# Performance work log

Measured on AMD Instinct MI355X. Metric: run time of the kernel, lower is better.

## Reference

```python
import jax, jax.numpy as jnp
import numpy as np

TIM_SIZE, TIM_EMB = 48, 64
APP_SIZE, APP_EMB = 10000, 256
UID_SIZE, UID_EMB = 10000, 256
INPUT_SIZE = TIM_EMB + APP_EMB  # 320
S = 4096
N = S - 3  # windows of length 4


def setup_inputs() -> dict:
    key = jax.random.key(0)
    ks = jax.random.split(key, 12)
    inp = {
        "tim": jax.random.randint(ks[0], (S, 1), 0, TIM_SIZE),
        "app": jax.random.uniform(ks[1], (S, APP_SIZE), dtype=jnp.float32),
        "loc": jax.random.randint(ks[2], (S, 1), 0, 1),
        "uid": jax.random.randint(ks[3], (1,), 0, UID_SIZE),
        "ptim": jax.random.randint(ks[4], (N, 1), 0, TIM_SIZE),
        # learned parameters
        "emb_tim_w": jax.random.normal(ks[5], (TIM_SIZE, TIM_EMB), dtype=jnp.float32) * 0.02,
        "emb_uid_w": jax.random.normal(ks[6], (UID_SIZE, UID_EMB), dtype=jnp.float32) * 0.02,
        "emb_app_w": jax.random.normal(ks[7], (APP_SIZE, APP_EMB), dtype=jnp.float32) * 0.02,
        "attn_W": jax.random.uniform(ks[8], (INPUT_SIZE, 1), dtype=jnp.float32),
        "attn_b": jax.random.uniform(ks[9], (4, 1), dtype=jnp.float32),
        "attn_fc_w": jax.random.normal(ks[10], (APP_EMB, INPUT_SIZE), dtype=jnp.float32) * 0.02,
        "attn_fc_b": jnp.zeros((APP_EMB,), dtype=jnp.float32),
        "dec_w": jax.random.normal(ks[11], (APP_SIZE, APP_EMB + TIM_EMB), dtype=jnp.float32) * 0.02,
        "dec_b": jnp.zeros((APP_SIZE,), dtype=jnp.float32),
    }
    return inp


def reference(tim, app, loc, uid, ptim, emb_tim_w, emb_uid_w, emb_app_w,
              attn_W, attn_b, attn_fc_w, attn_fc_b, dec_w, dec_b):
    # embeddings (squeeze(1) in torch)
    tim_emb = emb_tim_w[tim[:, 0]]    # [S, TIM_EMB]
    ptim_emb = emb_tim_w[ptim[:, 0]]  # [N, TIM_EMB]
    # 'sum' app embedding mode: multi-hot @ table
    app_emb = app @ emb_app_w         # [S, APP_EMB]
    x = jnp.concatenate([app_emb, tim_emb], axis=1)  # [S, INPUT_SIZE]; dropout is identity at eval
    # sliding windows of length 4 (vectorizes the torch per-i loop)
    n = tim.shape[0] - 3
    idx = jnp.arange(n)[:, None] + jnp.arange(4)[None, :]  # [N, 4]
    win = x[idx]                                          # [N, 4, INPUT_SIZE]
    H = jnp.tanh(win @ attn_W + attn_b)                   # [N, 4, 1]
    Xn = H / jnp.sum(jnp.abs(H), axis=(1, 2), keepdims=True)  # L1 normalize over the window
    pooled = jnp.einsum('nf,nfd->nd', Xn[:, :, 0], win)   # [N, INPUT_SIZE]
    out = pooled @ attn_fc_w.T + attn_fc_b                # [N, APP_EMB]
    uid_emb = emb_uid_w[uid[0]]                           # [APP_EMB], broadcast = repeat
    out = out * uid_emb
    out = jnp.concatenate([out, ptim_emb], axis=1)        # [N, APP_EMB+TIM_EMB]
    score = jax.nn.sigmoid(out @ dec_w.T + dec_b)         # [N, APP_SIZE]
    return score
```

## Files before the change

kernel.cpp:

```cpp
#include <hip/hip_runtime.h>

typedef __attribute__((ext_vector_type(8))) short  bf16x8;
typedef __attribute__((ext_vector_type(8))) unsigned short u16x8;
typedef __attribute__((ext_vector_type(4))) float  f32x4;

constexpr int S    = 4096;
constexpr int NR   = 4093;
constexpr int KAPP = 10000;
constexpr int EAPP = 256;
constexpr int ETIM = 64;
constexpr int DIN  = 320;
constexpr int NDEC = 10000;
constexpr int NSK  = 10;
constexpr int KCH  = 1024;
constexpr int KPAD = NSK * KCH;
constexpr int NS   = KCH / 32;
constexpr int LDP  = 40;
constexpr int LDA2 = 328;

__device__ inline unsigned short f2bf(float f) {
    unsigned u = __float_as_uint(f);
    u += 0x7fffu + ((u >> 16) & 1u);
    return (unsigned short)(u >> 16);
}
__device__ inline float bf2f(unsigned short h) {
    return __uint_as_float(((unsigned)h) << 16);
}
__device__ inline u16x8 pack8(f32x4 a, f32x4 b) {
    u16x8 v;
    v[0]=f2bf(a.x); v[1]=f2bf(a.y); v[2]=f2bf(a.z); v[3]=f2bf(a.w);
    v[4]=f2bf(b.x); v[5]=f2bf(b.y); v[6]=f2bf(b.z); v[7]=f2bf(b.w);
    return v;
}
__device__ inline bf16x8 as_bf(u16x8 v) {
    union { u16x8 u; bf16x8 b; } c; c.u = v; return c.b;
}

__global__ __launch_bounds__(256) void k_cvt_bf16(
    const float* __restrict__ in, unsigned short* __restrict__ out, int n8)
{
    int id = blockIdx.x * 256 + threadIdx.x;
    if (id >= n8) return;
    const float* p = in + (size_t)id * 8;
    f32x4 a = *reinterpret_cast<const f32x4*>(p);
    f32x4 b = *reinterpret_cast<const f32x4*>(p + 4);
    *reinterpret_cast<u16x8*>(out + (size_t)id * 8) = pack8(a, b);
}

__global__ __launch_bounds__(256) void k_transpose_appw(
    const float* __restrict__ B, unsigned short* __restrict__ Bp)
{
    __shared__ float T[64][68];
    const int kt = blockIdx.x * 64, nt = blockIdx.y * 64;
    const int tid = threadIdx.x;
    #pragma unroll
    for (int i = 0; i < 4; ++i) {
        int c = tid + (i << 8);
        int k = c >> 4, n4 = (c & 15) << 2;
        f32x4 v = {0.f, 0.f, 0.f, 0.f};
        if (kt + k < KAPP)
            v = *reinterpret_cast<const f32x4*>(&B[(size_t)(kt + k) * EAPP + nt + n4]);
        *reinterpret_cast<f32x4*>(&T[k][n4]) = v;
    }
    __syncthreads();
    #pragma unroll
    for (int i = 0; i < 2; ++i) {
        int c = tid + (i << 8);
        int n = c >> 3, ko = (c & 7) << 3;
        u16x8 v;
        #pragma unroll
        for (int j = 0; j < 8; ++j) v[j] = f2bf(T[ko + j][n]);
        *reinterpret_cast<u16x8*>(&Bp[(size_t)(nt + n) * KPAD + kt + ko]) = v;
    }
}

__global__ __launch_bounds__(256) void k_embed_tim(
    const int* __restrict__ tim, const float* __restrict__ emb_tim,
    unsigned short* __restrict__ xb)
{
    int r = blockIdx.x * 4 + (threadIdx.x >> 6);
    int e = threadIdx.x & 63;
    xb[(size_t)r * DIN + EAPP + e] = f2bf(emb_tim[tim[r] * ETIM + e]);
}
__global__ __launch_bounds__(256) void k_embed_ptim(
    const int* __restrict__ ptim, const float* __restrict__ emb_tim,
    unsigned short* __restrict__ yb)
{
    int r = blockIdx.x * 4 + (threadIdx.x >> 6);
    int e = threadIdx.x & 63;
    if (r < NR) yb[(size_t)r * DIN + EAPP + e] = f2bf(emb_tim[ptim[r] * ETIM + e]);
}

__global__ __launch_bounds__(256, 3) void k_app(
    const float* __restrict__ A, const unsigned short* __restrict__ Bp,
    float* __restrict__ part)
{
    __shared__ unsigned short As[2][64 * LDP];
    __shared__ unsigned short Bs[2][256 * LDP];
    const int tid = threadIdx.x, lane = tid & 63, w = tid >> 6;
    const int ks = blockIdx.x, bm = blockIdx.y << 6;
    const int wc = w << 6, rl = lane & 15, kh8 = (lane >> 4) << 3;
    const int k0 = ks * KCH;
    const int arow = tid >> 2, ak0 = (tid & 3) << 3;

    u16x8 ra, rb[4];
    auto gload = [&](int step) {
        const int kt = k0 + (step << 5);
        {
            const int k = kt + ak0;
            u16x8 v = {0,0,0,0,0,0,0,0};
            if (k < KAPP) {
                const float* p = &A[(size_t)(bm + arow) * KAPP + k];
                v = pack8(*reinterpret_cast<const f32x4*>(p),
                          *reinterpret_cast<const f32x4*>(p + 4));
            }
            ra = v;
        }
        #pragma unroll
        for (int i = 0; i < 4; ++i) {
            int c = tid + (i << 8);
            int row = c >> 2, ko = (c & 3) << 3;
            rb[i] = *reinterpret_cast<const u16x8*>(&Bp[(size_t)row * KPAD + kt + ko]);
        }
    };
    auto swrite = [&](int b) {
        *reinterpret_cast<u16x8*>(&As[b][arow * LDP + ak0]) = ra;
        #pragma unroll
        for (int i = 0; i < 4; ++i) {
            int c = tid + (i << 8);
            int row = c >> 2, ko = (c & 3) << 3;
            *reinterpret_cast<u16x8*>(&Bs[b][row * LDP + ko]) = rb[i];
        }
    };

    f32x4 acc[4][4];
    #pragma unroll
    for (int i = 0; i < 4; ++i)
        #pragma unroll
        for (int j = 0; j < 4; ++j) acc[i][j] = (f32x4){0.f, 0.f, 0.f, 0.f};

    gload(0); swrite(0); __syncthreads();
    for (int t = 0; t < NS; ++t) {
        const int cur = t & 1;
        const bool more = (t + 1 < NS);
        if (more) gload(t + 1);
        bf16x8 af[4], bfr[4];
        #pragma unroll
        for (int i = 0; i < 4; ++i)
            af[i] = *reinterpret_cast<const bf16x8*>(
                &As[cur][(i * 16 + rl) * LDP + kh8]);
        #pragma unroll
        for (int j = 0; j < 4; ++j)
            bfr[j] = *reinterpret_cast<const bf16x8*>(
                &Bs[cur][(wc + j * 16 + rl) * LDP + kh8]);
        #pragma unroll
        for (int i = 0; i < 4; ++i)
            #pragma unroll
            for (int j = 0; j < 4; ++j)
                acc[i][j] = __builtin_amdgcn_mfma_f32_16x16x32_bf16(
                    af[i], bfr[j], acc[i][j], 0, 0, 0);
        if (more) swrite(cur ^ 1);
        __syncthreads();
    }

    float* P = part + ((size_t)ks * S + bm) * EAPP;
    const int rq = (lane >> 4) << 2;
    #pragma unroll
    for (int i = 0; i < 4; ++i)
        #pragma unroll
        for (int j = 0; j < 4; ++j) {
            int col = wc + j * 16 + rl;
            #pragma unroll
            for (int q = 0; q < 4; ++q)
                P[(size_t)(i * 16 + rq + q) * EAPP + col] = acc[i][j][q];
        }
}

__global__ __launch_bounds__(256) void k_reduce_app(
    const float* __restrict__ part, unsigned short* __restrict__ xb)
{
    int id = blockIdx.x * 256 + threadIdx.x;
    int row = id >> 6, c4 = (id & 63) << 2;
    f32x4 s = {0.f, 0.f, 0.f, 0.f};
    #pragma unroll
    for (int sl = 0; sl < NSK; ++sl) {
        f32x4 v = *reinterpret_cast<const f32x4*>(
            &part[((size_t)sl * S + row) * EAPP + c4]);
        s.x += v.x; s.y += v.y; s.z += v.z; s.w += v.w;
    }
    unsigned short* o = &xb[(size_t)row * DIN + c4];
    o[0] = f2bf(s.x); o[1] = f2bf(s.y); o[2] = f2bf(s.z); o[3] = f2bf(s.w);
}

__global__ __launch_bounds__(256) void k_score(
    const unsigned short* __restrict__ xb, const float* __restrict__ W,
    float* __restrict__ s)
{
    int wv = threadIdx.x >> 6, lane = threadIdx.x & 63;
    int m = blockIdx.x * 4 + wv;
    float sum = 0.f;
    #pragma unroll
    for (int i = 0; i < 5; ++i) {
        int k = lane + (i << 6);
        sum += bf2f(xb[(size_t)m * DIN + k]) * W[k];
    }
    #pragma unroll
    for (int off = 32; off; off >>= 1) sum += __shfl_down(sum, off);
    if (lane == 0) s[m] = sum;
}

__global__ void k_pooled(
    const unsigned short* __restrict__ xb, const float* __restrict__ s,
    const float* __restrict__ attn_b, unsigned short* __restrict__ pooledb)
{
    int n = blockIdx.x, d = threadIdx.x;
    float h[4], den = 0.f;
    #pragma unroll
    for (int f = 0; f < 4; ++f) {
        h[f] = tanhf(s[n + f] + attn_b[f]);
        den += fabsf(h[f]);
    }
    float inv = 1.f / den, p = 0.f;
    #pragma unroll
    for (int f = 0; f < 4; ++f)
        p = fmaf(h[f] * inv, bf2f(xb[(size_t)(n + f) * DIN + d]), p);
    pooledb[(size_t)n * DIN + d] = f2bf(p);
}

template<int EPI>
__global__ __launch_bounds__(256, 3) void k_nt320(
    const unsigned short* __restrict__ A, const unsigned short* __restrict__ B,
    int Nb, int Mlim,
    const float* __restrict__ bias,
    const float* __restrict__ emb_uid, const int* __restrict__ uid,
    void* __restrict__ Cout, int ldc)
{
    __shared__ unsigned short As[64 * LDA2];
    const int tid = threadIdx.x, lane = tid & 63, w = tid >> 6;
    const int qx = gridDim.x >> 3;
    const int swz = (blockIdx.x & 7) * qx + (blockIdx.x >> 3);
    const int bm = (swz & 63) << 6, bn = (swz >> 6) << 8;
    const int rl = lane & 15, kh8 = (lane >> 4) << 3;
    const int wc = w << 6;

    {
        const int row = tid >> 2, c0 = tid & 3;
        const unsigned short* src = A + (size_t)(bm + row) * DIN;
        unsigned short* dst = As + row * LDA2;
        #pragma unroll
        for (int t = 0; t < 10; ++t) {
            int ch = (c0 + (t << 2)) << 3;
            *reinterpret_cast<u16x8*>(dst + ch) =
                *reinterpret_cast<const u16x8*>(src + ch);
        }
    }
    __syncthreads();

    f32x4 acc[4][4];
    #pragma unroll
    for (int i = 0; i < 4; ++i)
        #pragma unroll
        for (int j = 0; j < 4; ++j) acc[i][j] = (f32x4){0.f, 0.f, 0.f, 0.f};

    u16x8 b0[4], b1[4];
#define LOADB(DST, KSN) do {                                                    \
    const int kg_ = ((KSN) << 5) + kh8;                                         \
    _Pragma("unroll")                                                           \
    for (int j = 0; j < 4; ++j) {                                               \
        int brow = bn + wc + j * 16 + rl;                                       \
        u16x8 v_ = {0,0,0,0,0,0,0,0};                                           \
        if (brow < Nb)                                                          \
            v_ = *reinterpret_cast<const u16x8*>(&B[(size_t)brow * DIN + kg_]); \
        DST[j] = v_;                                                            \
    }                                                                           \
} while (0)

#define STEPNT(BARR, KSN) do {                                                  \
    const int kg_ = ((KSN) << 5) + kh8;                                         \
    bf16x8 af_[4];                                                              \
    _Pragma("unroll")                                                           \
    for (int i = 0; i < 4; ++i)                                                 \
        af_[i] = *reinterpret_cast<const bf16x8*>(                              \
            &As[(i * 16 + rl) * LDA2 + kg_]);                                   \
    _Pragma("unroll")                                                           \
    for (int i = 0; i < 4; ++i)                                                 \
        _Pragma("unroll")                                                       \
        for (int j = 0; j < 4; ++j)                                             \
            acc[i][j] = __builtin_amdgcn_mfma_f32_16x16x32_bf16(                \
                af_[i], as_bf(BARR[j]), acc[i][j], 0, 0, 0);                     \
} while (0)

    LOADB(b0, 0);
    #pragma unroll
    for (int p = 0; p < 5; ++p) {
        LOADB(b1, 2 * p + 1);
        STEPNT(b0, 2 * p);
        if (2 * p + 2 < 10) LOADB(b0, 2 * p + 2);
        STEPNT(b1, 2 * p + 1);
    }
#undef LOADB
#undef STEPNT

    const int rq = (lane >> 4) << 2;
    if (EPI == 1) {
        unsigned short* C = (unsigned short*)Cout;
        const float* us = emb_uid + (size_t)uid[0] * EAPP;
        #pragma unroll
        for (int j = 0; j < 4; ++j) {
            int col = bn + wc + j * 16 + rl;
            if (col >= Nb) continue;
            float um = us[col], bb = bias[col];
            #pragma unroll
            for (int i = 0; i < 4; ++i)
                #pragma unroll
                for (int q = 0; q < 4; ++q) {
                    int row = bm + i * 16 + rq + q;
                    if (row < Mlim)
                        C[(size_t)row * ldc + col] = f2bf((acc[i][j][q] + bb) * um);
                }
        }
    } else {
        float* C = (float*)Cout;
        #pragma unroll
        for (int j = 0; j < 4; ++j) {
            int col = bn + wc + j * 16 + rl;
            if (col >= Nb) continue;
            float bb = bias[col];
            #pragma unroll
            for (int i = 0; i < 4; ++i)
                #pragma unroll
                for (int q = 0; q < 4; ++q) {
                    int row = bm + i * 16 + rq + q;
                    if (row < Mlim) {
                        float v = acc[i][j][q] + bb;
                        C[(size_t)row * ldc + col] = 1.f / (1.f + __expf(-v));
                    }
                }
        }
    }
}

extern "C" void kernel_launch(void* const* d_in, const int* in_sizes, int n_in,
                              void* d_out, int out_size, void* d_ws, size_t ws_size,
                              hipStream_t stream)
{
    const int*   tim       = (const int*)  d_in[0];
    const float* app       = (const float*)d_in[1];
    const int*   uid       = (const int*)  d_in[3];
    const int*   ptim      = (const int*)  d_in[4];
    const float* emb_tim_w = (const float*)d_in[5];
    const float* emb_uid_w = (const float*)d_in[6];
    const float* emb_app_w = (const float*)d_in[7];
    const float* attn_W    = (const float*)d_in[8];
    const float* attn_b    = (const float*)d_in[9];
    const float* attn_fc_w = (const float*)d_in[10];
    const float* attn_fc_b = (const float*)d_in[11];
    const float* dec_w     = (const float*)d_in[12];
    const float* dec_b     = (const float*)d_in[13];
    float* out = (float*)d_out;

    char* w = (char*)d_ws;
    size_t o = 0;
    auto alloc = [&](size_t bytes) { char* p = w + o; o = (o + bytes + 511) & ~(size_t)511; return p; };
    unsigned short* xb      = (unsigned short*)alloc((size_t)S * DIN * 2);
    unsigned short* pooledb = (unsigned short*)alloc((size_t)S * DIN * 2);
    unsigned short* yb      = (unsigned short*)alloc((size_t)S * DIN * 2);
    float*          s       = (float*)        alloc((size_t)S * 4);
    unsigned short* Bp      = (unsigned short*)alloc((size_t)EAPP * KPAD * 2);
    unsigned short* decb    = (unsigned short*)alloc((size_t)NDEC * DIN * 2);
    unsigned short* fcb     = (unsigned short*)alloc((size_t)EAPP * DIN * 2);
    float*          part    = (float*)        alloc((size_t)NSK * S * EAPP * 4);

    k_cvt_bf16<<<(NDEC * DIN / 8 + 255) / 256, 256, 0, stream>>>(dec_w, decb, NDEC * DIN / 8);
    k_cvt_bf16<<<(EAPP * DIN / 8 + 255) / 256, 256, 0, stream>>>(attn_fc_w, fcb, EAPP * DIN / 8);
    dim3 gT(KPAD / 64, EAPP / 64);
    k_transpose_appw<<<gT, 256, 0, stream>>>(emb_app_w, Bp);
    k_embed_tim<<<S / 4, 256, 0, stream>>>(tim, emb_tim_w, xb);

    dim3 gApp(NSK, S / 64);
    k_app<<<gApp, 256, 0, stream>>>(app, Bp, part);
    k_reduce_app<<<S * 64 / 256, 256, 0, stream>>>(part, xb);

    k_score<<<S / 4, 256, 0, stream>>>(xb, attn_W, s);
    k_pooled<<<NR, DIN, 0, stream>>>(xb, s, attn_b, pooledb);
    k_embed_ptim<<<S / 4, 256, 0, stream>>>(ptim, emb_tim_w, yb);

    k_nt320<1><<<64, 256, 0, stream>>>(pooledb, fcb, EAPP, S,
                                       attn_fc_b, emb_uid_w, uid, yb, DIN);
    k_nt320<2><<<40 * 64, 256, 0, stream>>>(yb, decb, NDEC, NR,
                                            dec_b, nullptr, nullptr, out, NDEC);
}
```

Before: 248.8 us.

## Use k-chunk-major LDS layout, rebalance split-K, raise occupancy bounds

Replaces the padded row-major LDS tiles in the app GEMM and the 320-wide NT GEMM with a layout where each 8-element k-chunk is stored contiguously across rows. MFMA fragment reads then become conflict-free sequential 16-byte accesses, and the padding is no longer needed. The app GEMM split-K changes from 10x1024 to 8x1280, which cuts the number of partial sums to reduce. Both kernels raise launch_bounds min-blocks from 3 to 4, and the NT kernel prefetches B two steps ahead. The higher occupancy target may force register spills.

```diff
diff --git a/kernel.cpp b/kernel.cpp
--- a/kernel.cpp
+++ b/kernel.cpp
@@ -11,12 +11,10 @@
 constexpr int ETIM = 64;
 constexpr int DIN  = 320;
 constexpr int NDEC = 10000;
-constexpr int NSK  = 10;
-constexpr int KCH  = 1024;
+constexpr int NSK  = 8;
+constexpr int KCH  = 1280;
 constexpr int KPAD = NSK * KCH;
 constexpr int NS   = KCH / 32;
-constexpr int LDP  = 40;
-constexpr int LDA2 = 328;
 
 __device__ inline unsigned short f2bf(float f) {
     unsigned u = __float_as_uint(f);
@@ -91,23 +89,23 @@
     if (r < NR) yb[(size_t)r * DIN + EAPP + e] = f2bf(emb_tim[ptim[r] * ETIM + e]);
 }
 
-__global__ __launch_bounds__(256, 3) void k_app(
+__global__ __launch_bounds__(256, 4) void k_app(
     const float* __restrict__ A, const unsigned short* __restrict__ Bp,
     float* __restrict__ part)
 {
-    __shared__ unsigned short As[2][64 * LDP];
-    __shared__ unsigned short Bs[2][256 * LDP];
+    __shared__ unsigned short As[2][4 * 64 * 8];
+    __shared__ unsigned short Bs[2][4 * 256 * 8];
     const int tid = threadIdx.x, lane = tid & 63, w = tid >> 6;
     const int ks = blockIdx.x, bm = blockIdx.y << 6;
-    const int wc = w << 6, rl = lane & 15, kh8 = (lane >> 4) << 3;
+    const int wc = w << 6, rl = lane & 15, kq = lane >> 4;
     const int k0 = ks * KCH;
-    const int arow = tid >> 2, ak0 = (tid & 3) << 3;
+    const int arow = tid >> 2, ac = tid & 3;
 
     u16x8 ra, rb[4];
     auto gload = [&](int step) {
         const int kt = k0 + (step << 5);
         {
-            const int k = kt + ak0;
+            const int k = kt + (ac << 3);
             u16x8 v = {0,0,0,0,0,0,0,0};
             if (k < KAPP) {
                 const float* p = &A[(size_t)(bm + arow) * KAPP + k];
@@ -119,17 +117,18 @@
         #pragma unroll
         for (int i = 0; i < 4; ++i) {
             int c = tid + (i << 8);
-            int row = c >> 2, ko = (c & 3) << 3;
-            rb[i] = *reinterpret_cast<const u16x8*>(&Bp[(size_t)row * KPAD + kt + ko]);
+            int row = c >> 2, ck = c & 3;
+            rb[i] = *reinterpret_cast<const u16x8*>(
+                &Bp[(size_t)row * KPAD + kt + (ck << 3)]);
         }
     };
     auto swrite = [&](int b) {
-        *reinterpret_cast<u16x8*>(&As[b][arow * LDP + ak0]) = ra;
+        *reinterpret_cast<u16x8*>(&As[b][((ac << 6) + arow) << 3]) = ra;
         #pragma unroll
         for (int i = 0; i < 4; ++i) {
             int c = tid + (i << 8);
-            int row = c >> 2, ko = (c & 3) << 3;
-            *reinterpret_cast<u16x8*>(&Bs[b][row * LDP + ko]) = rb[i];
+            int row = c >> 2, ck = c & 3;
+            *reinterpret_cast<u16x8*>(&Bs[b][((ck << 8) + row) << 3]) = rb[i];
         }
     };
 
@@ -148,11 +147,11 @@
         #pragma unroll
         for (int i = 0; i < 4; ++i)
             af[i] = *reinterpret_cast<const bf16x8*>(
-                &As[cur][(i * 16 + rl) * LDP + kh8]);
+                &As[cur][((kq << 6) + i * 16 + rl) << 3]);
         #pragma unroll
         for (int j = 0; j < 4; ++j)
             bfr[j] = *reinterpret_cast<const bf16x8*>(
-                &Bs[cur][(wc + j * 16 + rl) * LDP + kh8]);
+                &Bs[cur][((kq << 8) + wc + j * 16 + rl) << 3]);
         #pragma unroll
         for (int i = 0; i < 4; ++i)
             #pragma unroll
@@ -164,7 +163,7 @@
     }
 
     float* P = part + ((size_t)ks * S + bm) * EAPP;
-    const int rq = (lane >> 4) << 2;
+    const int rq = kq << 2;
     #pragma unroll
     for (int i = 0; i < 4; ++i)
         #pragma unroll
@@ -228,30 +227,29 @@
 }
 
 template<int EPI>
-__global__ __launch_bounds__(256, 3) void k_nt320(
+__global__ __launch_bounds__(256, 4) void k_nt320(
     const unsigned short* __restrict__ A, const unsigned short* __restrict__ B,
     int Nb, int Mlim,
     const float* __restrict__ bias,
     const float* __restrict__ emb_uid, const int* __restrict__ uid,
     void* __restrict__ Cout, int ldc)
 {
-    __shared__ unsigned short As[64 * LDA2];
+    __shared__ unsigned short As[40 * 64 * 8];
     const int tid = threadIdx.x, lane = tid & 63, w = tid >> 6;
     const int qx = gridDim.x >> 3;
     const int swz = (blockIdx.x & 7) * qx + (blockIdx.x >> 3);
     const int bm = (swz & 63) << 6, bn = (swz >> 6) << 8;
-    const int rl = lane & 15, kh8 = (lane >> 4) << 3;
+    const int rl = lane & 15, kq = lane >> 4;
     const int wc = w << 6;
 
     {
         const int row = tid >> 2, c0 = tid & 3;
         const unsigned short* src = A + (size_t)(bm + row) * DIN;
-        unsigned short* dst = As + row * LDA2;
         #pragma unroll
         for (int t = 0; t < 10; ++t) {
-            int ch = (c0 + (t << 2)) << 3;
-            *reinterpret_cast<u16x8*>(dst + ch) =
-                *reinterpret_cast<const u16x8*>(src + ch);
+            int ck = c0 + (t << 2);
+            *reinterpret_cast<u16x8*>(&As[((ck << 6) + row) << 3]) =
+                *reinterpret_cast<const u16x8*>(src + (ck << 3));
         }
     }
     __syncthreads();
@@ -264,7 +262,7 @@
 
     u16x8 b0[4], b1[4];
 #define LOADB(DST, KSN) do {                                                    \
-    const int kg_ = ((KSN) << 5) + kh8;                                         \
+    const int kg_ = ((KSN) << 5) + (kq << 3);                                   \
     _Pragma("unroll")                                                           \
     for (int j = 0; j < 4; ++j) {                                               \
         int brow = bn + wc + j * 16 + rl;                                       \
@@ -276,12 +274,12 @@
 } while (0)
 
 #define STEPNT(BARR, KSN) do {                                                  \
-    const int kg_ = ((KSN) << 5) + kh8;                                         \
+    const int ckb_ = (((KSN) << 2) + kq) << 6;                                  \
     bf16x8 af_[4];                                                              \
     _Pragma("unroll")                                                           \
     for (int i = 0; i < 4; ++i)                                                 \
         af_[i] = *reinterpret_cast<const bf16x8*>(                              \
-            &As[(i * 16 + rl) * LDA2 + kg_]);                                   \
+            &As[(ckb_ + i * 16 + rl) << 3]);                                    \
     _Pragma("unroll")                                                           \
     for (int i = 0; i < 4; ++i)                                                 \
         _Pragma("unroll")                                                       \
@@ -291,17 +289,18 @@
 } while (0)
 
     LOADB(b0, 0);
+    LOADB(b1, 1);
     #pragma unroll
     for (int p = 0; p < 5; ++p) {
-        LOADB(b1, 2 * p + 1);
         STEPNT(b0, 2 * p);
         if (2 * p + 2 < 10) LOADB(b0, 2 * p + 2);
         STEPNT(b1, 2 * p + 1);
+        if (2 * p + 3 < 10) LOADB(b1, 2 * p + 3);
     }
 #undef LOADB
 #undef STEPNT
 
-    const int rq = (lane >> 4) << 2;
+    const int rq = kq << 2;
     if (EPI == 1) {
         unsigned short* C = (unsigned short*)Cout;
         const float* us = emb_uid + (size_t)uid[0] * EAPP;
```

Measured after the change: 265.7 us. +6.8%, slower.
